# Kernel optimization log

Hardware: AMD Instinct MI355X
Metric: run time of the kernel (lower is better)

Reference implementation:

```python
import jax, jax.numpy as jnp
import numpy as np

B, S, D, H = 4, 1024, 1024, 16
HD = D // H  # head dim = 64
SCALE = 1.0 / float(np.sqrt(HD))
W_INIT = 0.02


def setup_inputs() -> dict:
    key = jax.random.key(0)
    ks = jax.random.split(key, 8)
    f = lambda k, shape: jax.random.normal(k, shape, dtype=jnp.float32)
    return {
        "q": f(ks[0], (B, S, D)),
        "k": f(ks[1], (B, S, D)),
        "v": f(ks[2], (B, S, D)),
        "Wq": f(ks[3], (D, D)) * W_INIT, "bq": jnp.zeros((D,), jnp.float32),
        "Wk": f(ks[4], (D, D)) * W_INIT, "bk": jnp.zeros((D,), jnp.float32),
        "Wv": f(ks[5], (D, D)) * W_INIT, "bv": jnp.zeros((D,), jnp.float32),
        "Wo": f(ks[6], (D, D)) * W_INIT, "bo": jnp.zeros((D,), jnp.float32),
    }


def _split_heads(x):
    # [B, S, D] -> [B, H, S, HD]
    return x.reshape(B, S, H, HD).transpose(0, 2, 1, 3)


def reference(q, k, v, Wq, bq, Wk, bk, Wv, bv, Wo, bo):
    # linear input projections (torch Linear: x @ W.T + b)
    qh = _split_heads(q @ Wq.T + bq) * SCALE
    kh = _split_heads(k @ Wk.T + bk)
    vh = _split_heads(v @ Wv.T + bv)
    # scaled dot-product attention, full score matrix as in the source
    scores = jnp.einsum("bhqd,bhkd->bhqk", qh, kh)  # [B,H,S,S]
    weights = jax.nn.softmax(scores, axis=-1)
    ctx = jnp.einsum("bhqk,bhkd->bhqd", weights, vh)  # [B,H,S,HD]
    ctx = ctx.transpose(0, 2, 1, 3).reshape(B, S, D)
    # output projection (dropout=0, activation=None -> identity)
    return ctx @ Wo.T + bo
```

## Files before the change

kernel.cpp:

```cpp
#include <hip/hip_runtime.h>
#include <hip/hip_bf16.h>

typedef __attribute__((ext_vector_type(8))) short short8;
typedef __attribute__((ext_vector_type(4))) float f32x4;

static __device__ __forceinline__ short f2bf(float x) {
    __hip_bfloat16 h(x);
    return __builtin_bit_cast(short, h);
}

static __device__ __forceinline__ void gload16(const void* g, void* l) {
    auto* gp = reinterpret_cast<const __attribute__((address_space(1))) unsigned*>(
        reinterpret_cast<uintptr_t>(g));
    auto* lp = reinterpret_cast<__attribute__((address_space(3))) unsigned*>(
        reinterpret_cast<uintptr_t>(l));
    __builtin_amdgcn_global_load_lds(gp, lp, 16, 0, 0);
}

__global__ __launch_bounds__(256) void convert_all(
    const float* __restrict__ q, const float* __restrict__ k, const float* __restrict__ v,
    const float* __restrict__ Wq, const float* __restrict__ Wk,
    const float* __restrict__ Wv, const float* __restrict__ Wo,
    short* __restrict__ abf_q, short* __restrict__ abf_k, short* __restrict__ abf_v,
    short* __restrict__ wbf)
{
    const int blk = blockIdx.x;
    const float* src;
    short* dst;
    size_t off;
    if (blk < 6144) {
        const int seg = blk >> 11;
        src = (seg == 0) ? q : (seg == 1) ? k : v;
        dst = (seg == 0) ? abf_q : (seg == 1) ? abf_k : abf_v;
        off = ((size_t)(blk & 2047) * 256 + threadIdx.x) * 8;
    } else {
        const int wseg = (blk - 6144) >> 9;
        src = (wseg == 0) ? Wq : (wseg == 1) ? Wk : (wseg == 2) ? Wv : Wo;
        dst = wbf + (size_t)wseg * 1048576;
        off = ((size_t)((blk - 6144) & 511) * 256 + threadIdx.x) * 8;
    }
    float4 f0 = *(const float4*)(src + off);
    float4 f1 = *(const float4*)(src + off + 4);
    short8 o;
    o[0] = f2bf(f0.x); o[1] = f2bf(f0.y); o[2] = f2bf(f0.z); o[3] = f2bf(f0.w);
    o[4] = f2bf(f1.x); o[5] = f2bf(f1.y); o[6] = f2bf(f1.z); o[7] = f2bf(f1.w);
    *(short8*)(dst + off) = o;
}

__global__ __launch_bounds__(256) void proj_qkv_kernel(
    const short* __restrict__ abf_q, const short* __restrict__ abf_k,
    const short* __restrict__ abf_v, const short* __restrict__ wbf,
    const float* __restrict__ bq, const float* __restrict__ bk, const float* __restrict__ bv,
    short* __restrict__ qh, short* __restrict__ kh, short* __restrict__ vt)
{
    const int z = blockIdx.z;
    const short* A    = (z == 0) ? abf_q : (z == 1) ? abf_k : abf_v;
    const short* W    = wbf + (size_t)z * 1048576;
    const float* bias = (z == 0) ? bq : (z == 1) ? bk : bv;

    __shared__ __align__(16) short As[128 * 64];
    __shared__ __align__(16) short Bs[128 * 64];

    const int tid = threadIdx.x;
    const int lane = tid & 63;
    const int w = tid >> 6;
    const int wr = w >> 1, wc = w & 1;
    const int row0 = blockIdx.x * 128;
    const int col0 = blockIdx.y * 128;
    const int fr = lane & 15;
    const int g = lane >> 4;
    const int frs = fr & 7;
    const int srow = lane >> 3;
    const int sch  = ((lane & 7) ^ srow) * 8;

    f32x4 acc[4][4] = {};

    for (int t = 0; t < 16; ++t) {
        const int k0 = t * 64;
        #pragma unroll
        for (int i = 0; i < 4; ++i) {
            const int r0 = w * 32 + i * 8;
            gload16(A + (size_t)(row0 + r0 + srow) * 1024 + k0 + sch, &As[r0 * 64]);
            gload16(W + (size_t)(col0 + r0 + srow) * 1024 + k0 + sch, &Bs[r0 * 64]);
        }
        __syncthreads();
        #pragma unroll
        for (int kk = 0; kk < 2; ++kk) {
            short8 aF[4], bF[4];
            #pragma unroll
            for (int m = 0; m < 4; ++m)
                aF[m] = *(const short8*)&As[(wr * 64 + m * 16 + fr) * 64 + (((kk * 4 + g) ^ frs) * 8)];
            #pragma unroll
            for (int n = 0; n < 4; ++n)
                bF[n] = *(const short8*)&Bs[(wc * 64 + n * 16 + fr) * 64 + (((kk * 4 + g) ^ frs) * 8)];
            if (z == 2) {
                #pragma unroll
                for (int m = 0; m < 4; ++m)
                    #pragma unroll
                    for (int n = 0; n < 4; ++n)
                        acc[m][n] = __builtin_amdgcn_mfma_f32_16x16x32_bf16(bF[n], aF[m], acc[m][n], 0, 0, 0);
            } else {
                #pragma unroll
                for (int m = 0; m < 4; ++m)
                    #pragma unroll
                    for (int n = 0; n < 4; ++n)
                        acc[m][n] = __builtin_amdgcn_mfma_f32_16x16x32_bf16(aF[m], bF[n], acc[m][n], 0, 0, 0);
            }
        }
        __syncthreads();
    }

    if (z == 2) {
        #pragma unroll
        for (int n = 0; n < 4; ++n) {
            #pragma unroll
            for (int i = 0; i < 4; ++i) {
                const int c = col0 + wc * 64 + n * 16 + g * 4 + i;
                const int h = c >> 6, hd = c & 63;
                const float bb = bias[c];
                #pragma unroll
                for (int m = 0; m < 4; ++m) {
                    const int r = row0 + wr * 64 + m * 16 + fr;
                    const int b = r >> 10, s = r & 1023;
                    vt[(((size_t)(b * 16 + h) * 64 + hd) << 10) + s] = f2bf(acc[m][n][i] + bb);
                }
            }
        }
    } else {
        short* out = (z == 0) ? qh : kh;
        const float scale = (z == 0) ? 0.1803368801111244f : 1.0f;
        #pragma unroll
        for (int n = 0; n < 4; ++n) {
            const int c = col0 + wc * 64 + n * 16 + fr;
            const int h = c >> 6, hd = c & 63;
            const float bb = bias[c];
            #pragma unroll
            for (int m = 0; m < 4; ++m) {
                #pragma unroll
                for (int i = 0; i < 4; ++i) {
                    const int r = row0 + wr * 64 + m * 16 + g * 4 + i;
                    const int b = r >> 10, s = r & 1023;
                    out[(((size_t)(b * 16 + h) * 1024 + s) << 6) + hd] =
                        f2bf((acc[m][n][i] + bb) * scale);
                }
            }
        }
    }
}

__global__ __launch_bounds__(256) void proj_o_kernel(
    const short* __restrict__ ctx, const short* __restrict__ wo,
    const float* __restrict__ bo, float* __restrict__ out)
{
    __shared__ __align__(16) short As[128 * 64];
    __shared__ __align__(16) short Bs[64 * 64];

    const int tid = threadIdx.x;
    const int lane = tid & 63;
    const int w = tid >> 6;
    const int row0 = blockIdx.x * 128;
    const int col0 = blockIdx.y * 64;
    const int fr = lane & 15;
    const int g = lane >> 4;
    const int frs = fr & 7;
    const int srow = lane >> 3;
    const int sch  = ((lane & 7) ^ srow) * 8;

    f32x4 acc[2][4] = {};

    for (int t = 0; t < 16; ++t) {
        const int k0 = t * 64;
        #pragma unroll
        for (int i = 0; i < 4; ++i) {
            const int r0 = w * 32 + i * 8;
            gload16(ctx + (size_t)(row0 + r0 + srow) * 1024 + k0 + sch, &As[r0 * 64]);
        }
        #pragma unroll
        for (int i = 0; i < 2; ++i) {
            const int r0 = w * 16 + i * 8;
            gload16(wo + (size_t)(col0 + r0 + srow) * 1024 + k0 + sch, &Bs[r0 * 64]);
        }
        __syncthreads();
        #pragma unroll
        for (int kk = 0; kk < 2; ++kk) {
            short8 aF[2], bF[4];
            #pragma unroll
            for (int m = 0; m < 2; ++m)
                aF[m] = *(const short8*)&As[(w * 32 + m * 16 + fr) * 64 + (((kk * 4 + g) ^ frs) * 8)];
            #pragma unroll
            for (int n = 0; n < 4; ++n)
                bF[n] = *(const short8*)&Bs[(n * 16 + fr) * 64 + (((kk * 4 + g) ^ frs) * 8)];
            #pragma unroll
            for (int m = 0; m < 2; ++m)
                #pragma unroll
                for (int n = 0; n < 4; ++n)
                    acc[m][n] = __builtin_amdgcn_mfma_f32_16x16x32_bf16(aF[m], bF[n], acc[m][n], 0, 0, 0);
        }
        __syncthreads();
    }

    #pragma unroll
    for (int n = 0; n < 4; ++n) {
        const int c = col0 + n * 16 + fr;
        const float bb = bo[c];
        #pragma unroll
        for (int m = 0; m < 2; ++m) {
            #pragma unroll
            for (int i = 0; i < 4; ++i) {
                const int r = row0 + w * 32 + m * 16 + g * 4 + i;
                out[(size_t)r * 1024 + c] = acc[m][n][i] + bb;
            }
        }
    }
}

__global__ __launch_bounds__(256) void attn_kernel(
    const short* __restrict__ qh, const short* __restrict__ kh,
    const short* __restrict__ vt, short* __restrict__ ctx)
{
    const int d = blockIdx.x;
    const int xcd = d & 7;
    const int s2 = d >> 3;
    const int bh = xcd * 8 + (s2 >> 3);
    const int qb = s2 & 7;
    const int b = bh >> 4, h = bh & 15;
    const int q0 = qb * 128;
    const short* Qh  = qh + (size_t)bh * 65536;
    const short* Kh  = kh + (size_t)bh * 65536;
    const short* Vth = vt + (size_t)bh * 65536;

    __shared__ __align__(16) short Ks[2][64 * 64];
    __shared__ __align__(16) short Vs[2][64 * 64];
    __shared__ __align__(16) short Pb[4][2][16 * 68];

    const int tid = threadIdx.x;
    const int lane = tid & 63;
    const int w = tid >> 6;
    const int fr = lane & 15;
    const int g = lane >> 4;
    const int fk = g * 8;
    const int srow = lane >> 3;
    const int sch  = ((lane & 7) ^ srow) * 8;

    short8 qF[2][2];
    #pragma unroll
    for (int m = 0; m < 2; ++m)
        #pragma unroll
        for (int j = 0; j < 2; ++j)
            qF[m][j] = *(const short8*)(Qh + (q0 + w * 32 + m * 16 + fr) * 64 + j * 32 + fk);

    short8 onesF;
    #pragma unroll
    for (int j = 0; j < 8; ++j) onesF[j] = (short)0x3F80;

    f32x4 o[2][4] = {};
    f32x4 lacc[2] = {};

    #pragma unroll
    for (int i = 0; i < 2; ++i) {
        const int r0 = w * 16 + i * 8;
        gload16(Kh + (size_t)(r0 + srow) * 64 + sch, &Ks[0][r0 * 64]);
        gload16(Vth + (size_t)(r0 + srow) * 1024 + sch, &Vs[0][r0 * 64]);
    }
    __syncthreads();

    for (int kt = 0; kt < 16; ++kt) {
        const int cur = kt & 1;
        if (kt < 15) {
            const int kv1 = (kt + 1) * 64;
            #pragma unroll
            for (int i = 0; i < 2; ++i) {
                const int r0 = w * 16 + i * 8;
                gload16(Kh + (size_t)(kv1 + r0 + srow) * 64 + sch, &Ks[cur ^ 1][r0 * 64]);
                gload16(Vth + (size_t)(r0 + srow) * 1024 + kv1 + sch, &Vs[cur ^ 1][r0 * 64]);
            }
        }

        f32x4 sc[2][4] = {};
        __builtin_amdgcn_s_setprio(1);
        #pragma unroll
        for (int n = 0; n < 4; ++n) {
            const int r = n * 16 + fr;
            #pragma unroll
            for (int j = 0; j < 2; ++j) {
                short8 kF = *(const short8*)&Ks[cur][r * 64 + (((j * 4 + g) ^ (fr & 7)) * 8)];
                #pragma unroll
                for (int m = 0; m < 2; ++m)
                    sc[m][n] = __builtin_amdgcn_mfma_f32_16x16x32_bf16(qF[m][j], kF, sc[m][n], 0, 0, 0);
            }
        }
        __builtin_amdgcn_s_setprio(0);

        #pragma unroll
        for (int m = 0; m < 2; ++m)
            #pragma unroll
            for (int n = 0; n < 4; ++n)
                #pragma unroll
                for (int i = 0; i < 4; ++i)
                    Pb[w][m][(g * 4 + i) * 68 + n * 16 + fr] = f2bf(exp2f(sc[m][n][i]));

        __builtin_amdgcn_s_setprio(1);
        #pragma unroll
        for (int half = 0; half < 2; ++half) {
            short8 pF[2];
            #pragma unroll
            for (int m = 0; m < 2; ++m)
                pF[m] = *(const short8*)&Pb[w][m][fr * 68 + half * 32 + fk];
            #pragma unroll
            for (int m = 0; m < 2; ++m)
                lacc[m] = __builtin_amdgcn_mfma_f32_16x16x32_bf16(pF[m], onesF, lacc[m], 0, 0, 0);
            #pragma unroll
            for (int n = 0; n < 4; ++n) {
                short8 vF = *(const short8*)&Vs[cur][(n * 16 + fr) * 64 + (((half * 4 + g) ^ (fr & 7)) * 8)];
                #pragma unroll
                for (int m = 0; m < 2; ++m)
                    o[m][n] = __builtin_amdgcn_mfma_f32_16x16x32_bf16(pF[m], vF, o[m][n], 0, 0, 0);
            }
        }
        __builtin_amdgcn_s_setprio(0);
        __syncthreads();
    }

    #pragma unroll
    for (int m = 0; m < 2; ++m) {
        float inv[4];
        #pragma unroll
        for (int i = 0; i < 4; ++i) inv[i] = 1.0f / lacc[m][i];
        #pragma unroll
        for (int n = 0; n < 4; ++n)
            #pragma unroll
            for (int i = 0; i < 4; ++i) {
                const int s = q0 + w * 32 + m * 16 + g * 4 + i;
                ctx[(size_t)(b * 1024 + s) * 1024 + h * 64 + n * 16 + fr] = f2bf(o[m][n][i] * inv[i]);
            }
    }
}

extern "C" void kernel_launch(void* const* d_in, const int* in_sizes, int n_in,
                              void* d_out, int out_size, void* d_ws, size_t ws_size,
                              hipStream_t stream) {
    const float* q  = (const float*)d_in[0];
    const float* k  = (const float*)d_in[1];
    const float* v  = (const float*)d_in[2];
    const float* Wq = (const float*)d_in[3];
    const float* bq = (const float*)d_in[4];
    const float* Wk = (const float*)d_in[5];
    const float* bk = (const float*)d_in[6];
    const float* Wv = (const float*)d_in[7];
    const float* bv = (const float*)d_in[8];
    const float* Wo = (const float*)d_in[9];
    const float* bo = (const float*)d_in[10];

    char* ws = (char*)d_ws;
    const size_t SZ = (size_t)4096 * 1024 * 2;
    short* qh    = (short*)(ws);
    short* kh    = (short*)(ws + SZ);
    short* vt    = (short*)(ws + 2 * SZ);
    short* ctx   = (short*)(ws + 3 * SZ);
    short* abf_v = (short*)(ws + 4 * SZ);
    short* wbf   = (short*)(ws + 5 * SZ);
    short* abf_q = (short*)d_out;
    short* abf_k = (short*)d_out + 4194304;

    convert_all<<<8192, 256, 0, stream>>>(q, k, v, Wq, Wk, Wv, Wo,
                                          abf_q, abf_k, abf_v, wbf);
    proj_qkv_kernel<<<dim3(32, 8, 3), 256, 0, stream>>>(
        abf_q, abf_k, abf_v, wbf, bq, bk, bv, qh, kh, vt);
    attn_kernel<<<512, 256, 0, stream>>>(qh, kh, vt, ctx);
    proj_o_kernel<<<dim3(32, 16), 256, 0, stream>>>(ctx, wbf + 3 * 1048576, bo, (float*)d_out);
}
```

Before: 207.6 us.

## Halve attention query tile, drop K/V double buffering, pack bf16 conversion

The attention kernel now processes 64 query rows per block instead of 128 and launches twice as many blocks. Each wave handles one 16-row fragment. The double-buffered K/V prefetch is replaced by a single buffer loaded synchronously each iteration, which roughly halves LDS use per block. Softmax probabilities are converted with packed v_cvt_pk_bf16_f32. The aim is more blocks and higher occupancy across CUs, at the cost of reloading K/V twice as often and losing overlap of global loads with compute.

```diff
diff --git a/kernel.cpp b/kernel.cpp
--- a/kernel.cpp
+++ b/kernel.cpp
@@ -15,6 +15,12 @@
     auto* lp = reinterpret_cast<__attribute__((address_space(3))) unsigned*>(
         reinterpret_cast<uintptr_t>(l));
     __builtin_amdgcn_global_load_lds(gp, lp, 16, 0, 0);
+}
+
+static __device__ __forceinline__ unsigned cvt_pk_bf16(float lo, float hi) {
+    unsigned r;
+    asm("v_cvt_pk_bf16_f32 %0, %1, %2" : "=v"(r) : "v"(lo), "v"(hi));
+    return r;
 }
 
 __global__ __launch_bounds__(256) void convert_all(
@@ -221,17 +227,17 @@
     const int d = blockIdx.x;
     const int xcd = d & 7;
     const int s2 = d >> 3;
-    const int bh = xcd * 8 + (s2 >> 3);
-    const int qb = s2 & 7;
+    const int bh = xcd * 8 + (s2 >> 4);
+    const int qb = s2 & 15;
     const int b = bh >> 4, h = bh & 15;
-    const int q0 = qb * 128;
+    const int q0 = qb * 64;
     const short* Qh  = qh + (size_t)bh * 65536;
     const short* Kh  = kh + (size_t)bh * 65536;
     const short* Vth = vt + (size_t)bh * 65536;
 
-    __shared__ __align__(16) short Ks[2][64 * 64];
-    __shared__ __align__(16) short Vs[2][64 * 64];
-    __shared__ __align__(16) short Pb[4][2][16 * 68];
+    __shared__ __align__(16) short Ks[64 * 64];
+    __shared__ __align__(16) short Vs[64 * 64];
+    __shared__ __align__(16) short Pb[4][16 * 68];
 
     const int tid = threadIdx.x;
     const int lane = tid & 63;
@@ -239,101 +245,83 @@
     const int fr = lane & 15;
     const int g = lane >> 4;
     const int fk = g * 8;
+    const int frs = fr & 7;
     const int srow = lane >> 3;
     const int sch  = ((lane & 7) ^ srow) * 8;
 
-    short8 qF[2][2];
-    #pragma unroll
-    for (int m = 0; m < 2; ++m)
-        #pragma unroll
-        for (int j = 0; j < 2; ++j)
-            qF[m][j] = *(const short8*)(Qh + (q0 + w * 32 + m * 16 + fr) * 64 + j * 32 + fk);
+    short8 qF[2];
+    #pragma unroll
+    for (int j = 0; j < 2; ++j)
+        qF[j] = *(const short8*)(Qh + (q0 + w * 16 + fr) * 64 + j * 32 + fk);
 
     short8 onesF;
     #pragma unroll
     for (int j = 0; j < 8; ++j) onesF[j] = (short)0x3F80;
 
-    f32x4 o[2][4] = {};
-    f32x4 lacc[2] = {};
-
-    #pragma unroll
-    for (int i = 0; i < 2; ++i) {
-        const int r0 = w * 16 + i * 8;
-        gload16(Kh + (size_t)(r0 + srow) * 64 + sch, &Ks[0][r0 * 64]);
-        gload16(Vth + (size_t)(r0 + srow) * 1024 + sch, &Vs[0][r0 * 64]);
-    }
-    __syncthreads();
+    f32x4 o[4] = {};
+    f32x4 lacc = {};
 
     for (int kt = 0; kt < 16; ++kt) {
-        const int cur = kt & 1;
-        if (kt < 15) {
-            const int kv1 = (kt + 1) * 64;
-            #pragma unroll
-            for (int i = 0; i < 2; ++i) {
-                const int r0 = w * 16 + i * 8;
-                gload16(Kh + (size_t)(kv1 + r0 + srow) * 64 + sch, &Ks[cur ^ 1][r0 * 64]);
-                gload16(Vth + (size_t)(r0 + srow) * 1024 + kv1 + sch, &Vs[cur ^ 1][r0 * 64]);
-            }
-        }
-
-        f32x4 sc[2][4] = {};
+        const int kv0 = kt * 64;
+        __syncthreads();
+        #pragma unroll
+        for (int i = 0; i < 2; ++i) {
+            const int r0 = w * 16 + i * 8;
+            gload16(Kh + (size_t)(kv0 + r0 + srow) * 64 + sch, &Ks[r0 * 64]);
+            gload16(Vth + (size_t)(r0 + srow) * 1024 + kv0 + sch, &Vs[r0 * 64]);
+        }
+        __syncthreads();
+
+        f32x4 sc[4] = {};
         __builtin_amdgcn_s_setprio(1);
         #pragma unroll
         for (int n = 0; n < 4; ++n) {
             const int r = n * 16 + fr;
             #pragma unroll
             for (int j = 0; j < 2; ++j) {
-                short8 kF = *(const short8*)&Ks[cur][r * 64 + (((j * 4 + g) ^ (fr & 7)) * 8)];
-                #pragma unroll
-                for (int m = 0; m < 2; ++m)
-                    sc[m][n] = __builtin_amdgcn_mfma_f32_16x16x32_bf16(qF[m][j], kF, sc[m][n], 0, 0, 0);
+                short8 kF = *(const short8*)&Ks[r * 64 + (((j * 4 + g) ^ frs) * 8)];
+                sc[n] = __builtin_amdgcn_mfma_f32_16x16x32_bf16(qF[j], kF, sc[n], 0, 0, 0);
             }
         }
         __builtin_amdgcn_s_setprio(0);
 
-        #pragma unroll
-        for (int m = 0; m < 2; ++m)
-            #pragma unroll
-            for (int n = 0; n < 4; ++n)
-                #pragma unroll
-                for (int i = 0; i < 4; ++i)
-                    Pb[w][m][(g * 4 + i) * 68 + n * 16 + fr] = f2bf(exp2f(sc[m][n][i]));
+        {
+            short* pbase = &Pb[w][(g * 4) * 68 + fr];
+            #pragma unroll
+            for (int n = 0; n < 4; ++n) {
+                const unsigned u01 = cvt_pk_bf16(exp2f(sc[n][0]), exp2f(sc[n][1]));
+                const unsigned u23 = cvt_pk_bf16(exp2f(sc[n][2]), exp2f(sc[n][3]));
+                pbase[n * 16]       = (short)u01;
+                pbase[n * 16 + 68]  = (short)(u01 >> 16);
+                pbase[n * 16 + 136] = (short)u23;
+                pbase[n * 16 + 204] = (short)(u23 >> 16);
+            }
+        }
 
         __builtin_amdgcn_s_setprio(1);
         #pragma unroll
         for (int half = 0; half < 2; ++half) {
-            short8 pF[2];
-            #pragma unroll
-            for (int m = 0; m < 2; ++m)
-                pF[m] = *(const short8*)&Pb[w][m][fr * 68 + half * 32 + fk];
-            #pragma unroll
-            for (int m = 0; m < 2; ++m)
-                lacc[m] = __builtin_amdgcn_mfma_f32_16x16x32_bf16(pF[m], onesF, lacc[m], 0, 0, 0);
+            short8 pF = *(const short8*)&Pb[w][fr * 68 + half * 32 + fk];
+            lacc = __builtin_amdgcn_mfma_f32_16x16x32_bf16(pF, onesF, lacc, 0, 0, 0);
             #pragma unroll
             for (int n = 0; n < 4; ++n) {
-                short8 vF = *(const short8*)&Vs[cur][(n * 16 + fr) * 64 + (((half * 4 + g) ^ (fr & 7)) * 8)];
-                #pragma unroll
-                for (int m = 0; m < 2; ++m)
-                    o[m][n] = __builtin_amdgcn_mfma_f32_16x16x32_bf16(pF[m], vF, o[m][n], 0, 0, 0);
+                short8 vF = *(const short8*)&Vs[(n * 16 + fr) * 64 + (((half * 4 + g) ^ frs) * 8)];
+                o[n] = __builtin_amdgcn_mfma_f32_16x16x32_bf16(pF, vF, o[n], 0, 0, 0);
             }
         }
         __builtin_amdgcn_s_setprio(0);
-        __syncthreads();
-    }
-
-    #pragma unroll
-    for (int m = 0; m < 2; ++m) {
-        float inv[4];
-        #pragma unroll
-        for (int i = 0; i < 4; ++i) inv[i] = 1.0f / lacc[m][i];
-        #pragma unroll
-        for (int n = 0; n < 4; ++n)
-            #pragma unroll
-            for (int i = 0; i < 4; ++i) {
-                const int s = q0 + w * 32 + m * 16 + g * 4 + i;
-                ctx[(size_t)(b * 1024 + s) * 1024 + h * 64 + n * 16 + fr] = f2bf(o[m][n][i] * inv[i]);
-            }
-    }
+    }
+
+    float inv[4];
+    #pragma unroll
+    for (int i = 0; i < 4; ++i) inv[i] = 1.0f / lacc[i];
+    #pragma unroll
+    for (int n = 0; n < 4; ++n)
+        #pragma unroll
+        for (int i = 0; i < 4; ++i) {
+            const int s = q0 + w * 16 + g * 4 + i;
+            ctx[(size_t)(b * 1024 + s) * 1024 + h * 64 + n * 16 + fr] = f2bf(o[n][i] * inv[i]);
+        }
 }
 
 extern "C" void kernel_launch(void* const* d_in, const int* in_sizes, int n_in,
@@ -366,6 +354,6 @@
                                           abf_q, abf_k, abf_v, wbf);
     proj_qkv_kernel<<<dim3(32, 8, 3), 256, 0, stream>>>(
         abf_q, abf_k, abf_v, wbf, bq, bk, bv, qh, kh, vt);
-    attn_kernel<<<512, 256, 0, stream>>>(qh, kh, vt, ctx);
+    attn_kernel<<<1024, 256, 0, stream>>>(qh, kh, vt, ctx);
     proj_o_kernel<<<dim3(32, 16), 256, 0, stream>>>(ctx, wbf + 3 * 1048576, bo, (float*)d_out);
 }
```

After: 206.4 us. Within noise of the previous version (-0.6%).
